# Optimization experiments

Hardware: AMD Instinct MI355X
Metric: run time of the kernel (lower is better)

The kernel has to match this reference:

```python
import jax, jax.numpy as jnp
import numpy as np

TOP_K = 8
SCALE = 2.5  # moe_router_scaling_factor
EPS = 1e-20


def setup_inputs() -> dict:
    key = jax.random.key(0)
    k1, k2 = jax.random.split(key)
    B, S, H, E = 4, 4096, 4096, 64
    hidden_states = jax.random.normal(k1, (B, S, H), dtype=jnp.float32)
    gate_weight = jax.random.normal(k2, (E, H), dtype=jnp.float32) * 0.02
    router_bias = jnp.zeros((E,), dtype=jnp.float32)
    return {"hidden_states": hidden_states, "gate_weight": gate_weight, "router_bias": router_bias}


def reference(hidden_states, gate_weight, router_bias):
    B, S, H = hidden_states.shape
    x = hidden_states.reshape(-1, H).astype(jnp.float32)  # [T, H]
    # need_fp32_gate: fp32 matmul against gate weight transpose -> [T, E]
    logits = jnp.einsum('th,eh->te', x, gate_weight.astype(jnp.float32))
    gate_prob = jax.nn.sigmoid(logits)
    biased = gate_prob + router_bias[None, :]
    # topk on bias-shifted probs; weights gathered from UNbiased probs
    _, indices = jax.lax.top_k(biased, TOP_K)                       # [T, K]
    topk_prob = jnp.take_along_axis(gate_prob, indices, axis=1)     # [T, K]
    weights = topk_prob / (jnp.sum(topk_prob, axis=-1, keepdims=True) + EPS)
    weights = weights * SCALE
    return weights, indices
```

## Files before the change

kernel.cpp:

```cpp
#include <hip/hip_runtime.h>
#include <cmath>


typedef float f32x4 __attribute__((ext_vector_type(4)));
typedef short s16x8 __attribute__((ext_vector_type(8)));

#define E_DIM 64
#define KC 32
#define CH_BYTES 12288
#define STILE 4096
#define NPART 4
#define W3_OFF 0
#define HI_OFF (2u << 20)

__device__ __forceinline__ unsigned short f2bf(float f) {
  unsigned u = __float_as_uint(f);
  u += 0x7fffu + ((u >> 16) & 1u);
  return (unsigned short)(u >> 16);
}
__device__ __forceinline__ float bf2f(unsigned short s) {
  return __uint_as_float(((unsigned)s) << 16);
}

__global__ __launch_bounds__(256) void split_w(
    const float* __restrict__ w, unsigned char* __restrict__ w3, int Hdim)
{
  const int kpr = Hdim >> 4;
  const int g = blockIdx.x * 256 + threadIdx.x;
  const int e = g / kpr;
  const int k0 = (g - e * kpr) * 16;
  if (e >= E_DIM) return;

  const float* src = w + (size_t)e * Hdim + k0;
  float f[16];
#pragma unroll
  for (int i = 0; i < 4; ++i) {
    float4 v = *(const float4*)(src + i * 4);
    f[i*4+0] = v.x; f[i*4+1] = v.y; f[i*4+2] = v.z; f[i*4+3] = v.w;
  }
  unsigned short hs[16], ms[16], ls[16];
#pragma unroll
  for (int i = 0; i < 16; ++i) {
    unsigned short h = f2bf(f[i]);
    float r1 = f[i] - bf2f(h);
    unsigned short m = f2bf(r1);
    float r2 = r1 - bf2f(m);
    hs[i] = h; ms[i] = m; ls[i] = f2bf(r2);
  }
  const int c   = k0 >> 5;
  const int klb = (k0 & 31) * 2;
  const int swz = ((e >> 1) & 3) << 4;
  unsigned char* base = w3 + (size_t)c * CH_BYTES + (size_t)e * 64;

#define STORE_SPLIT(arr, s)                                             \
  do {                                                                  \
    _Pragma("unroll")                                                   \
    for (int h2 = 0; h2 < 2; ++h2) {                                    \
      s16x8 pack;                                                       \
      _Pragma("unroll")                                                 \
      for (int j = 0; j < 8; ++j) pack[j] = (short)arr[h2*8 + j];       \
      *(s16x8*)(base + (s)*STILE + ((klb + h2*16) ^ swz)) = pack;       \
    }                                                                   \
  } while (0)

  STORE_SPLIT(hs, 0);
  STORE_SPLIT(ms, 1);
  STORE_SPLIT(ls, 2);
#undef STORE_SPLIT
}

__global__ __launch_bounds__(256, 4) void router_mfma(
    const float* __restrict__ x, const unsigned char* __restrict__ w3,
    const float* __restrict__ bias, float* __restrict__ outw,
    float* __restrict__ outi, float* __restrict__ hi_p,
    float* __restrict__ lo_p, int T, int Hdim)
{
  __shared__ __align__(16) unsigned char lds[2][CH_BYTES];

  const int tid  = threadIdx.x;
  const int wid  = tid >> 6;
  const int lane = tid & 63;
  const int lc   = lane & 15;
  const int lq   = lane >> 4;
  const int t0   = blockIdx.x * 64;
  const int by   = blockIdx.y;
  const int nch  = Hdim / KC / gridDim.y;

  const unsigned char* w3p = w3 + (size_t)by * nch * CH_BYTES;
  const float* xp = x + (size_t)(t0 + wid * 16 + lc) * Hdim
                      + (size_t)by * nch * KC + lq * 8;

  f32x4 acc_m[4] = {{0,0,0,0},{0,0,0,0},{0,0,0,0},{0,0,0,0}};
  f32x4 acc_c[4] = {{0,0,0,0},{0,0,0,0},{0,0,0,0},{0,0,0,0}};
  f32x4 sum_[4]  = {{0,0,0,0},{0,0,0,0},{0,0,0,0},{0,0,0,0}};
  f32x4 comp[4]  = {{0,0,0,0},{0,0,0,0},{0,0,0,0},{0,0,0,0}};

  const int kbyte = (lq * 16) ^ (((lc >> 1) & 3) << 4);
  const int erow  = lc * 64;

#define STAGE(c, b)                                                          \
  do {                                                                       \
    const unsigned char* gs = w3p + (size_t)(c) * CH_BYTES + tid * 16;       \
    unsigned char* ld_ = &lds[b][0] + tid * 16;                              \
    _Pragma("unroll")                                                        \
    for (int i = 0; i < 3; ++i)                                              \
      __builtin_amdgcn_global_load_lds(                                      \
          (const __attribute__((address_space(1))) unsigned int*)(gs + i*4096), \
          (__attribute__((address_space(3))) unsigned int*)(ld_ + i*4096),   \
          16, 0, 0);                                                         \
  } while (0)

#define LOADX(c, xr)                                                         \
  do {                                                                       \
    const float* p_ = xp + (size_t)(c) * KC;                                 \
    xr[0] = *(const float4*)(p_);                                            \
    xr[1] = *(const float4*)(p_ + 4);                                        \
  } while (0)

#define COMPUTE(xr, b)                                                       \
  do {                                                                       \
    float fv[8] = {xr[0].x, xr[0].y, xr[0].z, xr[0].w,                       \
                   xr[1].x, xr[1].y, xr[1].z, xr[1].w};                      \
    s16x8 ah, am, al;                                                        \
    _Pragma("unroll")                                                        \
    for (int j = 0; j < 8; ++j) {                                            \
      unsigned short h_ = f2bf(fv[j]);                                       \
      float r1_ = fv[j] - bf2f(h_);                                          \
      unsigned short m_ = f2bf(r1_);                                         \
      float r2_ = r1_ - bf2f(m_);                                            \
      ah[j] = (short)h_; am[j] = (short)m_; al[j] = (short)f2bf(r2_);        \
    }                                                                        \
    const unsigned char* B_ = &lds[b][0];                                    \
    _Pragma("unroll")                                                        \
    for (int n = 0; n < 4; ++n) {                                            \
      const int ro_ = n * 1024 + erow + kbyte;                               \
      s16x8 bh = *(const s16x8*)(B_ + ro_);                                  \
      s16x8 bm = *(const s16x8*)(B_ + STILE + ro_);                          \
      s16x8 bl = *(const s16x8*)(B_ + 2*STILE + ro_);                        \
      acc_m[n] = __builtin_amdgcn_mfma_f32_16x16x32_bf16(ah, bh, acc_m[n], 0,0,0); \
      acc_c[n] = __builtin_amdgcn_mfma_f32_16x16x32_bf16(ah, bm, acc_c[n], 0,0,0); \
      acc_c[n] = __builtin_amdgcn_mfma_f32_16x16x32_bf16(am, bh, acc_c[n], 0,0,0); \
      acc_c[n] = __builtin_amdgcn_mfma_f32_16x16x32_bf16(ah, bl, acc_c[n], 0,0,0); \
      acc_c[n] = __builtin_amdgcn_mfma_f32_16x16x32_bf16(am, bm, acc_c[n], 0,0,0); \
      acc_c[n] = __builtin_amdgcn_mfma_f32_16x16x32_bf16(al, bh, acc_c[n], 0,0,0); \
    }                                                                        \
  } while (0)

#define FOLD()                                                               \
  do {                                                                       \
    _Pragma("unroll")                                                        \
    for (int n = 0; n < 4; ++n) {                                            \
      _Pragma("unroll")                                                      \
      for (int r = 0; r < 4; ++r) {                                          \
        float a_ = acc_m[n][r];                                              \
        float s_ = sum_[n][r];                                               \
        float t_ = s_ + a_;                                                  \
        float z_ = t_ - s_;                                                  \
        comp[n][r] += (s_ - (t_ - z_)) + (a_ - z_);                          \
        sum_[n][r] = t_;                                                     \
        acc_m[n][r] = 0.f;                                                   \
      }                                                                      \
    }                                                                        \
  } while (0)

  float4 xa[2], xb[2];

  STAGE(0, 0);
  LOADX(0, xa);
  __syncthreads();

#pragma unroll 1
  for (int c2 = 0; c2 < nch / 2; ++c2) {
    const int c = c2 * 2;
    STAGE(c + 1, 1);
    LOADX(c + 1, xb);
    COMPUTE(xa, 0);
    __syncthreads();
    if (c + 2 < nch) { STAGE(c + 2, 0); LOADX(c + 2, xa); }
    COMPUTE(xb, 1);
    __syncthreads();
    FOLD();
  }

  if (gridDim.y != 1) {
#pragma unroll
    for (int n = 0; n < 4; ++n)
#pragma unroll
      for (int r = 0; r < 4; ++r) {
        const int t = t0 + wid * 16 + lq * 4 + r;
        const size_t o = ((size_t)by * T + t) * E_DIM + n * 16 + lc;
        hi_p[o] = sum_[n][r];
        lo_p[o] = comp[n][r] + acc_c[n][r];
      }
    return;
  }

  float bias_v[4];
#pragma unroll
  for (int n = 0; n < 4; ++n) bias_v[n] = bias[n * 16 + lc];

  float pr[4][4], bi[4][4];
#pragma unroll
  for (int n = 0; n < 4; ++n)
#pragma unroll
    for (int r = 0; r < 4; ++r) {
      float logit = sum_[n][r] + (comp[n][r] + acc_c[n][r]);
      float p = 1.0f / (1.0f + expf(-logit));
      pr[n][r] = p;
      bi[n][r] = p + bias_v[n];
    }

#pragma unroll
  for (int r = 0; r < 4; ++r) {
    float v0 = bi[0][r], v1 = bi[1][r], v2 = bi[2][r], v3 = bi[3][r];
    float p0 = pr[0][r], p1 = pr[1][r], p2 = pr[2][r], p3 = pr[3][r];
    float sum = 0.f, selp = 0.f;
    int seli = 0;
#pragma unroll
    for (int k = 0; k < 8; ++k) {
      float bv = v0; int bn = 0; float bp = p0;
      if (v1 > bv) { bv = v1; bn = 1; bp = p1; }
      if (v2 > bv) { bv = v2; bn = 2; bp = p2; }
      if (v3 > bv) { bv = v3; bn = 3; bp = p3; }
      int be = bn * 16 + lc;
#pragma unroll
      for (int off = 8; off >= 1; off >>= 1) {
        float ov = __shfl_xor(bv, off);
        float op = __shfl_xor(bp, off);
        int   oe = __shfl_xor(be, off);
        if (ov > bv || (ov == bv && oe < be)) { bv = ov; bp = op; be = oe; }
      }
      sum += bp;
      if (lc == k) { selp = bp; seli = be; }
      if (lc == (be & 15)) {
        int gsel = be >> 4;
        if      (gsel == 0) v0 = -1e30f;
        else if (gsel == 1) v1 = -1e30f;
        else if (gsel == 2) v2 = -1e30f;
        else                v3 = -1e30f;
      }
    }
    if (lc < 8) {
      const int t = t0 + wid * 16 + lq * 4 + r;
      outw[(size_t)t * 8 + lc] = selp * 2.5f / (sum + 1e-20f);
      outi[(size_t)t * 8 + lc] = (float)seli;
    }
  }
}

__global__ __launch_bounds__(256) void router_topk(
    const float* __restrict__ hi_p, const float* __restrict__ lo_p,
    const float* __restrict__ bias, float* __restrict__ outw,
    float* __restrict__ outi, int T)
{
  const int lane = threadIdx.x & 63;
  const int t = blockIdx.x * 4 + (threadIdx.x >> 6);
  if (t >= T) return;

  float s = 0.f, c = 0.f, losum = 0.f;
#pragma unroll
  for (int p = 0; p < NPART; ++p) {
    const size_t o = ((size_t)p * T + t) * E_DIM + lane;
    float a = hi_p[o];
    float tt = s + a;
    float z = tt - s;
    c += (s - (tt - z)) + (a - z);
    s = tt;
    losum += lo_p[o];
  }
  const float logit = s + (c + losum);

  const float prob = 1.0f / (1.0f + expf(-logit));
  float v = prob + bias[lane];

  float sum = 0.f, selw = 0.f;
  int seli = 0;
#pragma unroll
  for (int k = 0; k < 8; ++k) {
    float rv = v;
    int   ri = lane;
#pragma unroll
    for (int off = 32; off > 0; off >>= 1) {
      float ov = __shfl_xor(rv, off);
      int   oi = __shfl_xor(ri, off);
      if (ov > rv || (ov == rv && oi < ri)) { rv = ov; ri = oi; }
    }
    float pwin = __shfl(prob, ri);
    sum += pwin;
    if (lane == k)  { selw = pwin; seli = ri; }
    if (lane == ri) v = -INFINITY;
  }

  if (lane < 8) {
    float scale = 2.5f / (sum + 1e-20f);
    outw[(size_t)t * 8 + lane] = selw * scale;
    outi[(size_t)t * 8 + lane] = (float)seli;
  }
}

extern "C" void kernel_launch(void* const* d_in, const int* in_sizes, int n_in,
                              void* d_out, int out_size, void* d_ws, size_t ws_size,
                              hipStream_t stream) {
  const float* x    = (const float*)d_in[0];
  const float* w    = (const float*)d_in[1];
  const float* bias = (const float*)d_in[2];

  const int E    = in_sizes[2];
  const int Hdim = in_sizes[1] / E;
  const int T    = in_sizes[0] / Hdim;

  unsigned char* ws = (unsigned char*)d_ws;
  unsigned char* w3 = ws + W3_OFF;
  float* hi_p = (float*)(ws + HI_OFF);
  float* lo_p = hi_p + (size_t)NPART * T * E_DIM;

  const size_t need = (size_t)HI_OFF + (size_t)2 * NPART * T * E_DIM * sizeof(float);
  const int nparts = (ws_size >= need) ? NPART : 1;

  const int nElemGroups = E * Hdim / 16;
  split_w<<<(nElemGroups + 255) / 256, 256, 0, stream>>>(w, w3, Hdim);

  float* outw = (float*)d_out;
  float* outi = outw + (size_t)T * 8;

  dim3 gridG(T / 64, nparts);
  router_mfma<<<gridG, 256, 0, stream>>>(x, w3, bias, outw, outi, hi_p, lo_p, T, Hdim);

  if (nparts != 1) {
    router_topk<<<(T + 3) / 4, 256, 0, stream>>>(hi_p, lo_p, bias, outw, outi, T);
  }
}
```

Before: 114.6 us.

## Load split weights directly to registers and process two token tiles per wave

Drops the LDS staging and barriers for the split bf16 weights. The weight layout is rewritten so each lane reads its MFMA B fragments straight from global memory. Each wave now handles 32 tokens instead of 16, so every weight fragment is reused across two token tiles. The grid is halved and launch bounds are set to 2 blocks per CU. The main and correction accumulators are merged into one and folded every two iterations. This adds register pressure and relies on L2/L1 for weight reuse across waves, and merging the accumulators may slightly change numerical behaviour.

```diff
diff --git a/kernel.cpp b/kernel.cpp
--- a/kernel.cpp
+++ b/kernel.cpp
@@ -8,9 +8,7 @@
 #define E_DIM 64
 #define KC 32
 #define CH_BYTES 12288
-#define STILE 4096
 #define NPART 4
-#define W3_OFF 0
 #define HI_OFF (2u << 20)
 
 __device__ __forceinline__ unsigned short f2bf(float f) {
@@ -47,20 +45,18 @@
     float r2 = r1 - bf2f(m);
     hs[i] = h; ms[i] = m; ls[i] = f2bf(r2);
   }
-  const int c   = k0 >> 5;
-  const int klb = (k0 & 31) * 2;
-  const int swz = ((e >> 1) & 3) << 4;
-  unsigned char* base = w3 + (size_t)c * CH_BYTES + (size_t)e * 64;
-
-#define STORE_SPLIT(arr, s)                                             \
-  do {                                                                  \
-    _Pragma("unroll")                                                   \
-    for (int h2 = 0; h2 < 2; ++h2) {                                    \
-      s16x8 pack;                                                       \
-      _Pragma("unroll")                                                 \
-      for (int j = 0; j < 8; ++j) pack[j] = (short)arr[h2*8 + j];       \
-      *(s16x8*)(base + (s)*STILE + ((klb + h2*16) ^ swz)) = pack;       \
-    }                                                                   \
+  const int c  = k0 >> 5;
+  const int n  = e >> 4;
+  const int la = (e & 15) + (((k0 & 31) >> 3) << 4);
+  unsigned char* base = w3 + (size_t)c * CH_BYTES + n * 1024;
+
+#define STORE_SPLIT(arr, s)                                              \
+  do {                                                                   \
+    s16x8 pa, pb;                                                        \
+    _Pragma("unroll")                                                    \
+    for (int j = 0; j < 8; ++j) { pa[j] = (short)arr[j]; pb[j] = (short)arr[8+j]; } \
+    *(s16x8*)(base + (s)*4096 + la * 16)        = pa;                    \
+    *(s16x8*)(base + (s)*4096 + (la + 16) * 16) = pb;                    \
   } while (0)
 
   STORE_SPLIT(hs, 0);
@@ -69,181 +65,185 @@
 #undef STORE_SPLIT
 }
 
-__global__ __launch_bounds__(256, 4) void router_mfma(
+__global__ __launch_bounds__(256, 2) void router_mfma(
     const float* __restrict__ x, const unsigned char* __restrict__ w3,
     const float* __restrict__ bias, float* __restrict__ outw,
     float* __restrict__ outi, float* __restrict__ hi_p,
     float* __restrict__ lo_p, int T, int Hdim)
 {
-  __shared__ __align__(16) unsigned char lds[2][CH_BYTES];
-
   const int tid  = threadIdx.x;
   const int wid  = tid >> 6;
   const int lane = tid & 63;
   const int lc   = lane & 15;
   const int lq   = lane >> 4;
-  const int t0   = blockIdx.x * 64;
   const int by   = blockIdx.y;
   const int nch  = Hdim / KC / gridDim.y;
-
-  const unsigned char* w3p = w3 + (size_t)by * nch * CH_BYTES;
-  const float* xp = x + (size_t)(t0 + wid * 16 + lc) * Hdim
-                      + (size_t)by * nch * KC + lq * 8;
-
-  f32x4 acc_m[4] = {{0,0,0,0},{0,0,0,0},{0,0,0,0},{0,0,0,0}};
-  f32x4 acc_c[4] = {{0,0,0,0},{0,0,0,0},{0,0,0,0},{0,0,0,0}};
-  f32x4 sum_[4]  = {{0,0,0,0},{0,0,0,0},{0,0,0,0},{0,0,0,0}};
-  f32x4 comp[4]  = {{0,0,0,0},{0,0,0,0},{0,0,0,0},{0,0,0,0}};
-
-  const int kbyte = (lq * 16) ^ (((lc >> 1) & 3) << 4);
-  const int erow  = lc * 64;
-
-#define STAGE(c, b)                                                          \
+  const int t0w  = blockIdx.x * 128 + wid * 32;
+
+  const float* x0 = x + (size_t)(t0w + lc) * Hdim + (size_t)by * nch * KC + lq * 8;
+  const float* x1 = x0 + (size_t)16 * Hdim;
+  const unsigned char* wb = w3 + (size_t)by * nch * CH_BYTES + lane * 16;
+
+  f32x4 acc[2][4];
+  f32x4 sum_[2][4];
+  f32x4 comp[2][4];
+#pragma unroll
+  for (int t = 0; t < 2; ++t)
+#pragma unroll
+    for (int n = 0; n < 4; ++n) {
+      acc[t][n] = (f32x4){0,0,0,0};
+      sum_[t][n] = (f32x4){0,0,0,0};
+      comp[t][n] = (f32x4){0,0,0,0};
+    }
+
+#define LOADB(c, B)                                                          \
   do {                                                                       \
-    const unsigned char* gs = w3p + (size_t)(c) * CH_BYTES + tid * 16;       \
-    unsigned char* ld_ = &lds[b][0] + tid * 16;                              \
+    const unsigned char* p_ = wb + (size_t)(c) * CH_BYTES;                   \
     _Pragma("unroll")                                                        \
-    for (int i = 0; i < 3; ++i)                                              \
-      __builtin_amdgcn_global_load_lds(                                      \
-          (const __attribute__((address_space(1))) unsigned int*)(gs + i*4096), \
-          (__attribute__((address_space(3))) unsigned int*)(ld_ + i*4096),   \
-          16, 0, 0);                                                         \
-  } while (0)
-
-#define LOADX(c, xr)                                                         \
+    for (int s = 0; s < 3; ++s) {                                            \
+      const unsigned char* ps_ = p_ + s * 4096;                              \
+      _Pragma("unroll")                                                      \
+      for (int n = 0; n < 4; ++n)                                            \
+        B[s*4+n] = *(const s16x8*)(ps_ + n * 1024);                          \
+    }                                                                        \
+  } while (0)
+
+#define LOADX(c, X)                                                          \
   do {                                                                       \
-    const float* p_ = xp + (size_t)(c) * KC;                                 \
-    xr[0] = *(const float4*)(p_);                                            \
-    xr[1] = *(const float4*)(p_ + 4);                                        \
-  } while (0)
-
-#define COMPUTE(xr, b)                                                       \
+    X[0] = *(const float4*)(x0 + (size_t)(c) * KC);                          \
+    X[1] = *(const float4*)(x0 + (size_t)(c) * KC + 4);                      \
+    X[2] = *(const float4*)(x1 + (size_t)(c) * KC);                          \
+    X[3] = *(const float4*)(x1 + (size_t)(c) * KC + 4);                      \
+  } while (0)
+
+#define COMPUTE(X, B)                                                        \
   do {                                                                       \
-    float fv[8] = {xr[0].x, xr[0].y, xr[0].z, xr[0].w,                       \
-                   xr[1].x, xr[1].y, xr[1].z, xr[1].w};                      \
-    s16x8 ah, am, al;                                                        \
     _Pragma("unroll")                                                        \
-    for (int j = 0; j < 8; ++j) {                                            \
-      unsigned short h_ = f2bf(fv[j]);                                       \
-      float r1_ = fv[j] - bf2f(h_);                                          \
-      unsigned short m_ = f2bf(r1_);                                         \
-      float r2_ = r1_ - bf2f(m_);                                            \
-      ah[j] = (short)h_; am[j] = (short)m_; al[j] = (short)f2bf(r2_);        \
-    }                                                                        \
-    const unsigned char* B_ = &lds[b][0];                                    \
-    _Pragma("unroll")                                                        \
-    for (int n = 0; n < 4; ++n) {                                            \
-      const int ro_ = n * 1024 + erow + kbyte;                               \
-      s16x8 bh = *(const s16x8*)(B_ + ro_);                                  \
-      s16x8 bm = *(const s16x8*)(B_ + STILE + ro_);                          \
-      s16x8 bl = *(const s16x8*)(B_ + 2*STILE + ro_);                        \
-      acc_m[n] = __builtin_amdgcn_mfma_f32_16x16x32_bf16(ah, bh, acc_m[n], 0,0,0); \
-      acc_c[n] = __builtin_amdgcn_mfma_f32_16x16x32_bf16(ah, bm, acc_c[n], 0,0,0); \
-      acc_c[n] = __builtin_amdgcn_mfma_f32_16x16x32_bf16(am, bh, acc_c[n], 0,0,0); \
-      acc_c[n] = __builtin_amdgcn_mfma_f32_16x16x32_bf16(ah, bl, acc_c[n], 0,0,0); \
-      acc_c[n] = __builtin_amdgcn_mfma_f32_16x16x32_bf16(am, bm, acc_c[n], 0,0,0); \
-      acc_c[n] = __builtin_amdgcn_mfma_f32_16x16x32_bf16(al, bh, acc_c[n], 0,0,0); \
+    for (int t = 0; t < 2; ++t) {                                            \
+      float fv[8] = {X[t*2].x, X[t*2].y, X[t*2].z, X[t*2].w,                 \
+                     X[t*2+1].x, X[t*2+1].y, X[t*2+1].z, X[t*2+1].w};        \
+      s16x8 ah, am, al;                                                      \
+      _Pragma("unroll")                                                      \
+      for (int j = 0; j < 8; ++j) {                                          \
+        unsigned short h_ = f2bf(fv[j]);                                     \
+        float r1_ = fv[j] - bf2f(h_);                                        \
+        unsigned short m_ = f2bf(r1_);                                       \
+        float r2_ = r1_ - bf2f(m_);                                          \
+        ah[j] = (short)h_; am[j] = (short)m_; al[j] = (short)f2bf(r2_);      \
+      }                                                                      \
+      _Pragma("unroll")                                                      \
+      for (int n = 0; n < 4; ++n) {                                          \
+        acc[t][n] = __builtin_amdgcn_mfma_f32_16x16x32_bf16(ah, B[n],   acc[t][n], 0,0,0); \
+        acc[t][n] = __builtin_amdgcn_mfma_f32_16x16x32_bf16(ah, B[4+n], acc[t][n], 0,0,0); \
+        acc[t][n] = __builtin_amdgcn_mfma_f32_16x16x32_bf16(am, B[n],   acc[t][n], 0,0,0); \
+        acc[t][n] = __builtin_amdgcn_mfma_f32_16x16x32_bf16(ah, B[8+n], acc[t][n], 0,0,0); \
+        acc[t][n] = __builtin_amdgcn_mfma_f32_16x16x32_bf16(am, B[4+n], acc[t][n], 0,0,0); \
+        acc[t][n] = __builtin_amdgcn_mfma_f32_16x16x32_bf16(al, B[n],   acc[t][n], 0,0,0); \
+      }                                                                      \
     }                                                                        \
   } while (0)
 
 #define FOLD()                                                               \
   do {                                                                       \
     _Pragma("unroll")                                                        \
-    for (int n = 0; n < 4; ++n) {                                            \
+    for (int t = 0; t < 2; ++t)                                              \
       _Pragma("unroll")                                                      \
-      for (int r = 0; r < 4; ++r) {                                          \
-        float a_ = acc_m[n][r];                                              \
-        float s_ = sum_[n][r];                                               \
-        float t_ = s_ + a_;                                                  \
-        float z_ = t_ - s_;                                                  \
-        comp[n][r] += (s_ - (t_ - z_)) + (a_ - z_);                          \
-        sum_[n][r] = t_;                                                     \
-        acc_m[n][r] = 0.f;                                                   \
-      }                                                                      \
-    }                                                                        \
-  } while (0)
-
-  float4 xa[2], xb[2];
-
-  STAGE(0, 0);
-  LOADX(0, xa);
-  __syncthreads();
+      for (int n = 0; n < 4; ++n)                                            \
+        _Pragma("unroll")                                                    \
+        for (int r = 0; r < 4; ++r) {                                        \
+          float a_ = acc[t][n][r];                                           \
+          float s_ = sum_[t][n][r];                                          \
+          float t_ = s_ + a_;                                                \
+          float z_ = t_ - s_;                                                \
+          comp[t][n][r] += (s_ - (t_ - z_)) + (a_ - z_);                     \
+          sum_[t][n][r] = t_;                                                \
+          acc[t][n][r] = 0.f;                                                \
+        }                                                                    \
+  } while (0)
+
+  float4 XA[4], XB[4];
+  LOADX(0, XA);
 
 #pragma unroll 1
-  for (int c2 = 0; c2 < nch / 2; ++c2) {
-    const int c = c2 * 2;
-    STAGE(c + 1, 1);
-    LOADX(c + 1, xb);
-    COMPUTE(xa, 0);
-    __syncthreads();
-    if (c + 2 < nch) { STAGE(c + 2, 0); LOADX(c + 2, xa); }
-    COMPUTE(xb, 1);
-    __syncthreads();
-    FOLD();
-  }
+  for (int c = 0; c < nch; c += 2) {
+    s16x8 BA[12];
+    LOADB(c, BA);
+    LOADX(c + 1, XB);
+    COMPUTE(XA, BA);
+    s16x8 BB[12];
+    LOADB(c + 1, BB);
+    if (c + 2 < nch) LOADX(c + 2, XA);
+    COMPUTE(XB, BB);
+    if ((c & 2) == 2) FOLD();
+  }
+  FOLD();
 
   if (gridDim.y != 1) {
 #pragma unroll
+    for (int t = 0; t < 2; ++t)
+#pragma unroll
+      for (int n = 0; n < 4; ++n)
+#pragma unroll
+        for (int r = 0; r < 4; ++r) {
+          const int tok = t0w + t * 16 + lq * 4 + r;
+          const size_t o = ((size_t)by * T + tok) * E_DIM + n * 16 + lc;
+          hi_p[o] = sum_[t][n][r];
+          lo_p[o] = comp[t][n][r];
+        }
+    return;
+  }
+
+  float bias_v[4];
+#pragma unroll
+  for (int n = 0; n < 4; ++n) bias_v[n] = bias[n * 16 + lc];
+
+#pragma unroll
+  for (int t = 0; t < 2; ++t) {
+    float pr[4][4], bi[4][4];
+#pragma unroll
     for (int n = 0; n < 4; ++n)
 #pragma unroll
       for (int r = 0; r < 4; ++r) {
-        const int t = t0 + wid * 16 + lq * 4 + r;
-        const size_t o = ((size_t)by * T + t) * E_DIM + n * 16 + lc;
-        hi_p[o] = sum_[n][r];
-        lo_p[o] = comp[n][r] + acc_c[n][r];
+        float logit = sum_[t][n][r] + comp[t][n][r];
+        float p = 1.0f / (1.0f + expf(-logit));
+        pr[n][r] = p;
+        bi[n][r] = p + bias_v[n];
       }
-    return;
-  }
-
-  float bias_v[4];
-#pragma unroll
-  for (int n = 0; n < 4; ++n) bias_v[n] = bias[n * 16 + lc];
-
-  float pr[4][4], bi[4][4];
-#pragma unroll
-  for (int n = 0; n < 4; ++n)
 #pragma unroll
     for (int r = 0; r < 4; ++r) {
-      float logit = sum_[n][r] + (comp[n][r] + acc_c[n][r]);
-      float p = 1.0f / (1.0f + expf(-logit));
-      pr[n][r] = p;
-      bi[n][r] = p + bias_v[n];
-    }
-
-#pragma unroll
-  for (int r = 0; r < 4; ++r) {
-    float v0 = bi[0][r], v1 = bi[1][r], v2 = bi[2][r], v3 = bi[3][r];
-    float p0 = pr[0][r], p1 = pr[1][r], p2 = pr[2][r], p3 = pr[3][r];
-    float sum = 0.f, selp = 0.f;
-    int seli = 0;
-#pragma unroll
-    for (int k = 0; k < 8; ++k) {
-      float bv = v0; int bn = 0; float bp = p0;
-      if (v1 > bv) { bv = v1; bn = 1; bp = p1; }
-      if (v2 > bv) { bv = v2; bn = 2; bp = p2; }
-      if (v3 > bv) { bv = v3; bn = 3; bp = p3; }
-      int be = bn * 16 + lc;
-#pragma unroll
-      for (int off = 8; off >= 1; off >>= 1) {
-        float ov = __shfl_xor(bv, off);
-        float op = __shfl_xor(bp, off);
-        int   oe = __shfl_xor(be, off);
-        if (ov > bv || (ov == bv && oe < be)) { bv = ov; bp = op; be = oe; }
+      float v0 = bi[0][r], v1 = bi[1][r], v2 = bi[2][r], v3 = bi[3][r];
+      float p0 = pr[0][r], p1 = pr[1][r], p2 = pr[2][r], p3 = pr[3][r];
+      float sum = 0.f, selp = 0.f;
+      int seli = 0;
+#pragma unroll
+      for (int k = 0; k < 8; ++k) {
+        float bv = v0; int bn = 0; float bp = p0;
+        if (v1 > bv) { bv = v1; bn = 1; bp = p1; }
+        if (v2 > bv) { bv = v2; bn = 2; bp = p2; }
+        if (v3 > bv) { bv = v3; bn = 3; bp = p3; }
+        int be = bn * 16 + lc;
+#pragma unroll
+        for (int off = 8; off >= 1; off >>= 1) {
+          float ov = __shfl_xor(bv, off);
+          float op = __shfl_xor(bp, off);
+          int   oe = __shfl_xor(be, off);
+          if (ov > bv || (ov == bv && oe < be)) { bv = ov; bp = op; be = oe; }
+        }
+        sum += bp;
+        if (lc == k) { selp = bp; seli = be; }
+        if (lc == (be & 15)) {
+          int gsel = be >> 4;
+          if      (gsel == 0) v0 = -1e30f;
+          else if (gsel == 1) v1 = -1e30f;
+          else if (gsel == 2) v2 = -1e30f;
+          else                v3 = -1e30f;
+        }
       }
-      sum += bp;
-      if (lc == k) { selp = bp; seli = be; }
-      if (lc == (be & 15)) {
-        int gsel = be >> 4;
-        if      (gsel == 0) v0 = -1e30f;
-        else if (gsel == 1) v1 = -1e30f;
-        else if (gsel == 2) v2 = -1e30f;
-        else                v3 = -1e30f;
+      if (lc < 8) {
+        const int tok = t0w + t * 16 + lq * 4 + r;
+        outw[(size_t)tok * 8 + lc] = selp * 2.5f / (sum + 1e-20f);
+        outi[(size_t)tok * 8 + lc] = (float)seli;
       }
-    }
-    if (lc < 8) {
-      const int t = t0 + wid * 16 + lq * 4 + r;
-      outw[(size_t)t * 8 + lc] = selp * 2.5f / (sum + 1e-20f);
-      outi[(size_t)t * 8 + lc] = (float)seli;
     }
   }
 }
@@ -310,7 +310,7 @@
   const int T    = in_sizes[0] / Hdim;
 
   unsigned char* ws = (unsigned char*)d_ws;
-  unsigned char* w3 = ws + W3_OFF;
+  unsigned char* w3 = ws;
   float* hi_p = (float*)(ws + HI_OFF);
   float* lo_p = hi_p + (size_t)NPART * T * E_DIM;
 
@@ -323,7 +323,7 @@
   float* outw = (float*)d_out;
   float* outi = outw + (size_t)T * 8;
 
-  dim3 gridG(T / 64, nparts);
+  dim3 gridG(T / 128, nparts);
   router_mfma<<<gridG, 256, 0, stream>>>(x, w3, bias, outw, outi, hi_p, lo_p, T, Hdim);
 
   if (nparts != 1) {
```

Result: slower. 126.2 us (+10.1%).
